# Kernel tuning notes

Hardware: AMD Instinct MI355X
Metric: run time of the kernel (lower is better)

## Reference

```python
import jax, jax.numpy as jnp
from jax import lax
import numpy as np

P, K1, K2 = 8, 5, 9  # nPaths, small/large ECA kernel sizes (from nDim=1024, nPaths=8)
LN_EPS = 1e-5


def setup_inputs() -> dict:
    key = jax.random.key(0)
    ks = jax.random.split(key, 6)
    b, c, l = 16, 1024, 4096
    return {
        "x": jax.random.normal(ks[0], (b, c, l), dtype=jnp.float32),
        "conv1_w": jax.random.normal(ks[1], (P, K1), dtype=jnp.float32) * 0.3,
        "conv2_w": jax.random.normal(ks[2], (P, K2), dtype=jnp.float32) * 0.3,
        "combine_w": jax.random.normal(ks[3], (2,), dtype=jnp.float32) * 0.5,
        "combine_b": jnp.zeros((), dtype=jnp.float32),
        "ln_g": jnp.ones((P,), dtype=jnp.float32),
        "ln_b": jnp.zeros((P,), dtype=jnp.float32),
        "W1": jax.random.normal(ks[4], (P, 2 * P), dtype=jnp.float32) * 0.3,
        "b1": jnp.zeros((2 * P,), dtype=jnp.float32),
        "W2": jax.random.normal(ks[5], (2 * P, P), dtype=jnp.float32) * 0.3,
        "b2": jnp.zeros((P,), dtype=jnp.float32),
    }


def _grouped_conv(y, w):
    # y: (b, P, D) pooled per-path features; w: (P, k) one 1-ch kernel per path.
    # Equivalent to the per-path Conv1d(1,1,k, padding=(k-1)//2) loop, fused.
    k = w.shape[-1]
    pad = (k - 1) // 2
    return lax.conv_general_dilated(
        y, w[:, None, :], window_strides=(1,), padding=[(pad, pad)],
        dimension_numbers=("NCH", "OIH", "NCH"), feature_group_count=y.shape[1])


def reference(x, conv1_w, conv2_w, combine_w, combine_b, ln_g, ln_b, W1, b1, W2, b2):
    b, c, l = x.shape
    nP = conv1_w.shape[0]
    D = c // nP
    pf = x.reshape(b, nP, D, l)          # (b, P, D, l)
    y = pf.mean(-1)                      # (b, P, D) global-avg-pool over l
    y1 = _grouped_conv(y, conv1_w)       # (b, P, D)
    y2 = _grouped_conv(y, conv2_w)       # (b, P, D)
    # combine = Conv1d(2,1,1): scalar mix of the two conv outputs + bias
    attn = jax.nn.sigmoid(combine_w[0] * y1 + combine_w[1] * y2 + combine_b)
    # cross-path gating MLP on per-path mean attention
    cross = attn.mean(-1)                # (b, P)
    mu = cross.mean(-1, keepdims=True)
    var = cross.var(-1, keepdims=True)   # biased, matches torch LayerNorm
    h = (cross - mu) / jnp.sqrt(var + LN_EPS) * ln_g + ln_b
    h = jax.nn.gelu(h @ W1 + b1, approximate=False)
    gate = jax.nn.sigmoid(h @ W2 + b2)   # (b, P)
    scale = attn * gate[:, :, None]      # (b, P, D)
    out = pf * scale[..., None]          # broadcast over l
    return out.reshape(b, c, l)
```

## Files before the change

### kernel.cpp

```cpp
#include <hip/hip_runtime.h>
#include <math.h>

#define NP 8
#define ND 128
#define NC 1024
#define NL 4096
#define NB 16
#define LN_EPS 1e-5f

#define NBLK 2048
#define NCHUNK 8
#define GRPS 64

typedef float v4f __attribute__((ext_vector_type(4)));

__device__ __forceinline__ float hsum(v4f v) { return v.x + v.y + v.z + v.w; }
__device__ __forceinline__ float sigmoid_f(float z) { return 1.f / (1.f + expf(-z)); }

__device__ __forceinline__ float gelu_f(float s) {
    const float t = 0.7978845608028654f * (s + 0.044715f * s * s * s);
    const float e = expf(2.f * t);
    return 0.5f * s * (1.f + (e - 1.f) / (e + 1.f));
}

__global__ __launch_bounds__(256, 8) void fused_kernel(
    const float* __restrict__ x, float* __restrict__ y,
    unsigned* __restrict__ garr, unsigned* __restrict__ grel,
    unsigned* __restrict__ root,
    const float* __restrict__ conv1_w, const float* __restrict__ conv2_w,
    const float* __restrict__ combine_w, const float* __restrict__ combine_b,
    const float* __restrict__ ln_g, const float* __restrict__ ln_b,
    const float* __restrict__ W1, const float* __restrict__ b1,
    const float* __restrict__ W2, const float* __restrict__ b2,
    float* __restrict__ out)
{
    const int tid    = threadIdx.x;
    const int bid    = blockIdx.x;
    const int grp    = bid >> 5;
    const bool lead  = (bid & 31) == 0;

    __shared__ float sred[4];
    __shared__ float sy[NC];
    __shared__ float sattn[NC];
    __shared__ float scross[NP];
    __shared__ float sh[NP];
    __shared__ float sh2[2 * NP];
    __shared__ float sgate[NP];
    __shared__ float sml[2];

    const size_t rstride = (size_t)NBLK * (NL / 4);

    const v4f* xb = (const v4f*)x + (size_t)bid * (NL / 4);
    v4f* ob       = (v4f*)out    + (size_t)bid * (NL / 4);

    v4f a0 = xb[tid], a1 = xb[tid + 256], a2 = xb[tid + 512], a3 = xb[tid + 768];
    v4f n0, n1, n2, n3;

    for (int c = 0; c < NCHUNK; ++c) {
        const int rowc = c * NBLK + bid;
        const int b    = rowc >> 10;
        const int ch0  = rowc & (NC - 1);

        {
            float ps = hsum(a0) + hsum(a1) + hsum(a2) + hsum(a3);
            ps += __shfl_down(ps, 32, 64); ps += __shfl_down(ps, 16, 64);
            ps += __shfl_down(ps, 8, 64);  ps += __shfl_down(ps, 4, 64);
            ps += __shfl_down(ps, 2, 64);  ps += __shfl_down(ps, 1, 64);
            if ((tid & 63) == 0) sred[tid >> 6] = ps;
        }
        __syncthreads();
        if (tid == 0) {
            const float ym = (sred[0] + sred[1] + sred[2] + sred[3]) * (1.f / NL);
            __hip_atomic_store(&y[rowc], ym, __ATOMIC_RELAXED, __HIP_MEMORY_SCOPE_AGENT);
            unsigned old = __hip_atomic_fetch_add(&garr[grp], 1u,
                              __ATOMIC_RELEASE, __HIP_MEMORY_SCOPE_AGENT);
            if (old == (unsigned)(c * 32 + 31))
                __hip_atomic_fetch_add(root, 1u,
                              __ATOMIC_RELEASE, __HIP_MEMORY_SCOPE_AGENT);
        }

        if (c + 1 < NCHUNK) {
            const v4f* xn = xb + (size_t)(c + 1) * rstride;
            n0 = xn[tid]; n1 = xn[tid + 256]; n2 = xn[tid + 512]; n3 = xn[tid + 768];
        }

        if (tid == 0) {
            if (lead) {
                while (__hip_atomic_load(root, __ATOMIC_RELAXED,
                                         __HIP_MEMORY_SCOPE_AGENT) < (unsigned)((c + 1) * GRPS))
                    __builtin_amdgcn_s_sleep(4);
                __hip_atomic_store(&grel[grp], (unsigned)(c + 1),
                                   __ATOMIC_RELAXED, __HIP_MEMORY_SCOPE_AGENT);
            } else {
                while (__hip_atomic_load(&grel[grp], __ATOMIC_RELAXED,
                                         __HIP_MEMORY_SCOPE_AGENT) < (unsigned)(c + 1))
                    __builtin_amdgcn_s_sleep(4);
            }
        }
        __syncthreads();

        const float* yb = y + b * NC;
        #pragma unroll
        for (int k = 0; k < 4; ++k) {
            const int i = tid + 256 * k;
            sy[i] = __hip_atomic_load(&yb[i], __ATOMIC_RELAXED, __HIP_MEMORY_SCOPE_AGENT);
        }
        __syncthreads();
        #pragma unroll
        for (int k = 0; k < 4; ++k) {
            const int pos = tid + 256 * k;
            const int p = pos >> 7, d = pos & 127;
            const float* rowp = sy + p * ND;
            float c1 = 0.f;
            #pragma unroll
            for (int t = 0; t < 5; ++t) {
                int dd = d + t - 2;
                float v = (dd >= 0 && dd < ND) ? rowp[dd] : 0.f;
                c1 += conv1_w[p * 5 + t] * v;
            }
            float c2 = 0.f;
            #pragma unroll
            for (int t = 0; t < 9; ++t) {
                int dd = d + t - 4;
                float v = (dd >= 0 && dd < ND) ? rowp[dd] : 0.f;
                c2 += conv2_w[p * 9 + t] * v;
            }
            sattn[pos] = sigmoid_f(combine_w[0] * c1 + combine_w[1] * c2 + combine_b[0]);
        }
        __syncthreads();
        if (tid < 128) {
            const int p = tid >> 4, o = (tid & 15) * 8;
            float s = 0.f;
            #pragma unroll
            for (int j = 0; j < 8; ++j) s += sattn[p * ND + o + j];
            s += __shfl_down(s, 8, 16); s += __shfl_down(s, 4, 16);
            s += __shfl_down(s, 2, 16); s += __shfl_down(s, 1, 16);
            if ((tid & 15) == 0) scross[p] = s * (1.f / ND);
        }
        __syncthreads();
        if (tid == 0) {
            float mu = 0.f;
            #pragma unroll
            for (int pp = 0; pp < NP; ++pp) mu += scross[pp];
            mu *= (1.f / NP);
            float var = 0.f;
            #pragma unroll
            for (int pp = 0; pp < NP; ++pp) { float dl = scross[pp] - mu; var += dl * dl; }
            sml[0] = mu;
            sml[1] = rsqrtf(var * (1.f / NP) + LN_EPS);
        }
        __syncthreads();
        if (tid < NP)
            sh[tid] = (scross[tid] - sml[0]) * sml[1] * ln_g[tid] + ln_b[tid];
        __syncthreads();
        if (tid < 2 * NP) {
            float s = b1[tid];
            #pragma unroll
            for (int pp = 0; pp < NP; ++pp) s += sh[pp] * W1[pp * (2 * NP) + tid];
            sh2[tid] = gelu_f(s);
        }
        __syncthreads();
        if (tid < NP) {
            float s = b2[tid];
            #pragma unroll
            for (int j = 0; j < 2 * NP; ++j) s += sh2[j] * W2[j * NP + tid];
            sgate[tid] = sigmoid_f(s);
        }
        __syncthreads();

        {
            const float s = sattn[ch0] * sgate[ch0 >> 7];
            v4f* oc = ob + (size_t)c * rstride;
            __builtin_nontemporal_store(a0 * s, &oc[tid]);
            __builtin_nontemporal_store(a1 * s, &oc[tid + 256]);
            __builtin_nontemporal_store(a2 * s, &oc[tid + 512]);
            __builtin_nontemporal_store(a3 * s, &oc[tid + 768]);
        }
        a0 = n0; a1 = n1; a2 = n2; a3 = n3;
        __syncthreads();
    }
}

__global__ __launch_bounds__(256) void pool_kernel(const float* __restrict__ x,
                                                   float* __restrict__ y) {
    const int wid  = threadIdx.x >> 6;
    const int lane = threadIdx.x & 63;
    const int row  = blockIdx.x * 4 + wid;
    const v4f* xr = (const v4f*)(x + (size_t)row * NL);
    float s = 0.f;
    #pragma unroll
    for (int i = 0; i < 16; ++i) {
        v4f v = xr[lane + i * 64];
        s += v.x + v.y + v.z + v.w;
    }
    #pragma unroll
    for (int off = 32; off; off >>= 1) s += __shfl_down(s, off, 64);
    if (lane == 0) y[row] = s * (1.f / NL);
}

__global__ __launch_bounds__(1024) void attn_kernel(
    const float* __restrict__ y,
    const float* __restrict__ conv1_w, const float* __restrict__ conv2_w,
    const float* __restrict__ combine_w, const float* __restrict__ combine_b,
    const float* __restrict__ ln_g, const float* __restrict__ ln_b,
    const float* __restrict__ W1, const float* __restrict__ b1,
    const float* __restrict__ W2, const float* __restrict__ b2,
    float* __restrict__ scale)
{
    const int b = blockIdx.x;
    const int tid = threadIdx.x;
    const int p = tid >> 7;
    const int d = tid & 127;

    __shared__ float sy[NC];
    __shared__ float sattn[NC];
    __shared__ float sred[16];
    __shared__ float scross[NP];
    __shared__ float sh[NP];
    __shared__ float sh2[2 * NP];
    __shared__ float sgate[NP];
    __shared__ float sml[2];

    sy[tid] = y[b * NC + tid];
    __syncthreads();

    const float* rowp = sy + p * ND;
    float c1 = 0.f;
    #pragma unroll
    for (int t = 0; t < 5; ++t) {
        int dd = d + t - 2;
        float v = (dd >= 0 && dd < ND) ? rowp[dd] : 0.f;
        c1 += conv1_w[p * 5 + t] * v;
    }
    float c2 = 0.f;
    #pragma unroll
    for (int t = 0; t < 9; ++t) {
        int dd = d + t - 4;
        float v = (dd >= 0 && dd < ND) ? rowp[dd] : 0.f;
        c2 += conv2_w[p * 9 + t] * v;
    }
    const float a = sigmoid_f(combine_w[0] * c1 + combine_w[1] * c2 + combine_b[0]);
    sattn[tid] = a;

    float r = a;
    #pragma unroll
    for (int off = 32; off; off >>= 1) r += __shfl_down(r, off, 64);
    const int lane = tid & 63, wid = tid >> 6;
    if (lane == 0) sred[wid] = r;
    __syncthreads();

    if (tid == 0) {
        float mu = 0.f, var = 0.f;
        #pragma unroll
        for (int pp = 0; pp < NP; ++pp) {
            scross[pp] = (sred[2 * pp] + sred[2 * pp + 1]) * (1.f / ND);
            mu += scross[pp];
        }
        mu *= (1.f / NP);
        #pragma unroll
        for (int pp = 0; pp < NP; ++pp) { float dl = scross[pp] - mu; var += dl * dl; }
        sml[0] = mu;
        sml[1] = rsqrtf(var * (1.f / NP) + LN_EPS);
    }
    __syncthreads();
    if (tid < NP)
        sh[tid] = (scross[tid] - sml[0]) * sml[1] * ln_g[tid] + ln_b[tid];
    __syncthreads();
    if (tid < 2 * NP) {
        float s = b1[tid];
        #pragma unroll
        for (int pp = 0; pp < NP; ++pp) s += sh[pp] * W1[pp * (2 * NP) + tid];
        sh2[tid] = gelu_f(s);
    }
    __syncthreads();
    if (tid < NP) {
        float s = b2[tid];
        #pragma unroll
        for (int j = 0; j < 2 * NP; ++j) s += sh2[j] * W2[j * NP + tid];
        sgate[tid] = sigmoid_f(s);
    }
    __syncthreads();

    scale[b * NC + tid] = sattn[tid] * sgate[p];
}

__global__ __launch_bounds__(256) void scale_kernel(const float* __restrict__ x,
                                                    const float* __restrict__ scale,
                                                    float* __restrict__ out) {
    const v4f* xv = (const v4f*)x;
    v4f* ov = (v4f*)out;
    const size_t n = (size_t)NB * NC * (NL / 4);
    const size_t stride = (size_t)gridDim.x * blockDim.x;
    for (size_t i = (size_t)blockIdx.x * blockDim.x + threadIdx.x; i < n; i += stride) {
        const float s = scale[i >> 10];
        v4f v = xv[i];
        v *= s;
        __builtin_nontemporal_store(v, &ov[i]);
    }
}

extern "C" void kernel_launch(void* const* d_in, const int* in_sizes, int n_in,
                              void* d_out, int out_size, void* d_ws, size_t ws_size,
                              hipStream_t stream) {
    const float* x         = (const float*)d_in[0];
    const float* conv1_w   = (const float*)d_in[1];
    const float* conv2_w   = (const float*)d_in[2];
    const float* combine_w = (const float*)d_in[3];
    const float* combine_b = (const float*)d_in[4];
    const float* ln_g      = (const float*)d_in[5];
    const float* ln_b      = (const float*)d_in[6];
    const float* W1        = (const float*)d_in[7];
    const float* b1        = (const float*)d_in[8];
    const float* W2        = (const float*)d_in[9];
    const float* b2        = (const float*)d_in[10];
    float* out = (float*)d_out;

    float* y        = (float*)d_ws;
    float* scale    = y + NB * NC;
    unsigned* garr  = (unsigned*)(void*)scale;
    unsigned* grel  = garr + GRPS;
    unsigned* root  = grel + GRPS;

    hipMemsetAsync((void*)garr, 0, (2 * GRPS + 16) * sizeof(unsigned), stream);

    int nb = 0;
    hipOccupancyMaxActiveBlocksPerMultiprocessor(&nb, fused_kernel, 256, 0);
    if (nb >= NBLK / 256) {
        void* args[] = { (void*)&x, (void*)&y, (void*)&garr, (void*)&grel, (void*)&root,
                         (void*)&conv1_w, (void*)&conv2_w,
                         (void*)&combine_w, (void*)&combine_b,
                         (void*)&ln_g, (void*)&ln_b,
                         (void*)&W1, (void*)&b1, (void*)&W2, (void*)&b2,
                         (void*)&out };
        hipLaunchCooperativeKernel((const void*)fused_kernel, dim3(NBLK), dim3(256),
                                   args, 0, stream);
    } else {
        pool_kernel<<<NB * NC / 4, 256, 0, stream>>>(x, y);
        attn_kernel<<<NB, 1024, 0, stream>>>(y, conv1_w, conv2_w, combine_w, combine_b,
                                             ln_g, ln_b, W1, b1, W2, b2, scale);
        scale_kernel<<<2048, 256, 0, stream>>>(x, scale, out);
    }
}
```

Baseline: 135.3 us.

## Process two rows per block chunk and re-read x instead of holding it in registers

The persistent fused kernel now handles two rows per block per chunk with half as many chunks, which halves the number of grid-wide barrier rounds. It drops the register-held current and prefetched rows and instead reads x again from memory for the scaling pass. This cuts synchronisation rounds and register pressure, but it doubles the reads of x, which on a 256MB input will mostly miss cache. It also removes the prefetch overlap across barriers.

```diff
diff --git a/kernel.cpp b/kernel.cpp
--- a/kernel.cpp
+++ b/kernel.cpp
@@ -9,7 +9,8 @@
 #define LN_EPS 1e-5f
 
 #define NBLK 2048
-#define NCHUNK 8
+#define NCHUNK 4
+#define RPC 2
 #define GRPS 64
 
 typedef float v4f __attribute__((ext_vector_type(4)));
@@ -39,7 +40,7 @@
     const int grp    = bid >> 5;
     const bool lead  = (bid & 31) == 0;
 
-    __shared__ float sred[4];
+    __shared__ float sred[RPC][4];
     __shared__ float sy[NC];
     __shared__ float sattn[NC];
     __shared__ float scross[NP];
@@ -48,43 +49,35 @@
     __shared__ float sgate[NP];
     __shared__ float sml[2];
 
-    const size_t rstride = (size_t)NBLK * (NL / 4);
-
-    const v4f* xb = (const v4f*)x + (size_t)bid * (NL / 4);
-    v4f* ob       = (v4f*)out    + (size_t)bid * (NL / 4);
-
-    v4f a0 = xb[tid], a1 = xb[tid + 256], a2 = xb[tid + 512], a3 = xb[tid + 768];
-    v4f n0, n1, n2, n3;
-
     for (int c = 0; c < NCHUNK; ++c) {
-        const int rowc = c * NBLK + bid;
-        const int b    = rowc >> 10;
-        const int ch0  = rowc & (NC - 1);
-
-        {
-            float ps = hsum(a0) + hsum(a1) + hsum(a2) + hsum(a3);
+        const int r0  = c * (NBLK * RPC) + RPC * bid;
+        const int b   = r0 >> 10;
+        const int ch0 = r0 & (NC - 1);
+        const v4f* x0 = (const v4f*)x + (size_t)r0 * (NL / 4);
+        v4f* o0       = (v4f*)out    + (size_t)r0 * (NL / 4);
+
+        #pragma unroll
+        for (int r = 0; r < RPC; ++r) {
+            const v4f* xr = x0 + (size_t)r * (NL / 4);
+            float ps = hsum(xr[tid]) + hsum(xr[tid + 256])
+                     + hsum(xr[tid + 512]) + hsum(xr[tid + 768]);
             ps += __shfl_down(ps, 32, 64); ps += __shfl_down(ps, 16, 64);
             ps += __shfl_down(ps, 8, 64);  ps += __shfl_down(ps, 4, 64);
             ps += __shfl_down(ps, 2, 64);  ps += __shfl_down(ps, 1, 64);
-            if ((tid & 63) == 0) sred[tid >> 6] = ps;
+            if ((tid & 63) == 0) sred[r][tid >> 6] = ps;
         }
         __syncthreads();
         if (tid == 0) {
-            const float ym = (sred[0] + sred[1] + sred[2] + sred[3]) * (1.f / NL);
-            __hip_atomic_store(&y[rowc], ym, __ATOMIC_RELAXED, __HIP_MEMORY_SCOPE_AGENT);
+            #pragma unroll
+            for (int r = 0; r < RPC; ++r) {
+                const float ym = (sred[r][0] + sred[r][1] + sred[r][2] + sred[r][3]) * (1.f / NL);
+                __hip_atomic_store(&y[r0 + r], ym, __ATOMIC_RELAXED, __HIP_MEMORY_SCOPE_AGENT);
+            }
             unsigned old = __hip_atomic_fetch_add(&garr[grp], 1u,
                               __ATOMIC_RELEASE, __HIP_MEMORY_SCOPE_AGENT);
             if (old == (unsigned)(c * 32 + 31))
                 __hip_atomic_fetch_add(root, 1u,
                               __ATOMIC_RELEASE, __HIP_MEMORY_SCOPE_AGENT);
-        }
-
-        if (c + 1 < NCHUNK) {
-            const v4f* xn = xb + (size_t)(c + 1) * rstride;
-            n0 = xn[tid]; n1 = xn[tid + 256]; n2 = xn[tid + 512]; n3 = xn[tid + 768];
-        }
-
-        if (tid == 0) {
             if (lead) {
                 while (__hip_atomic_load(root, __ATOMIC_RELAXED,
                                          __HIP_MEMORY_SCOPE_AGENT) < (unsigned)((c + 1) * GRPS))
@@ -168,15 +161,16 @@
         }
         __syncthreads();
 
-        {
-            const float s = sattn[ch0] * sgate[ch0 >> 7];
-            v4f* oc = ob + (size_t)c * rstride;
-            __builtin_nontemporal_store(a0 * s, &oc[tid]);
-            __builtin_nontemporal_store(a1 * s, &oc[tid + 256]);
-            __builtin_nontemporal_store(a2 * s, &oc[tid + 512]);
-            __builtin_nontemporal_store(a3 * s, &oc[tid + 768]);
-        }
-        a0 = n0; a1 = n1; a2 = n2; a3 = n3;
+        #pragma unroll
+        for (int r = 0; r < RPC; ++r) {
+            const float s = sattn[ch0 + r] * sgate[(ch0 + r) >> 7];
+            const v4f* xr = x0 + (size_t)r * (NL / 4);
+            v4f* orr      = o0 + (size_t)r * (NL / 4);
+            __builtin_nontemporal_store(xr[tid]       * s, &orr[tid]);
+            __builtin_nontemporal_store(xr[tid + 256] * s, &orr[tid + 256]);
+            __builtin_nontemporal_store(xr[tid + 512] * s, &orr[tid + 512]);
+            __builtin_nontemporal_store(xr[tid + 768] * s, &orr[tid + 768]);
+        }
         __syncthreads();
     }
 }
```

Result: no change. 137.3 us (+1.5%).
